# Performance work log

Hardware: AMD Instinct MI355X
Metric: run time of the kernel (lower is better)

## Reference

```python
import jax, jax.numpy as jnp
from jax import lax
import numpy as np

EPS = 1e-4  # ProtoPNet standard epsilon (undefined in simplified source; canonical value)


def setup_inputs() -> dict:
    key = jax.random.key(0)
    k1, k2, k3, k4 = jax.random.split(key, 4)
    B, C_in, H, W = 16, 3, 512, 512
    P, C, NUM_CLASSES = 190, 64, 19
    x = jax.random.normal(k1, (B, C_in, H, W), dtype=jnp.float32)
    feat_w = jax.random.normal(k2, (C, C_in, 7, 7), dtype=jnp.float32) * 0.05  # conv stem, stride 4
    feat_b = jnp.zeros((C,), dtype=jnp.float32)
    prototype_vectors = jax.random.normal(k3, (P, C, 1, 1), dtype=jnp.float32) * 0.1
    last_w = jax.random.normal(k4, (NUM_CLASSES, P), dtype=jnp.float32) * 0.1  # Linear, no bias
    return {"x": x, "feat_w": feat_w, "feat_b": feat_b,
            "prototype_vectors": prototype_vectors, "last_w": last_w}


def reference(x, feat_w, feat_b, prototype_vectors, last_w):
    # features backbone: Conv2d(3->64, k=7, s=4, p=3)
    f = lax.conv_general_dilated(
        x, feat_w, window_strides=(4, 4), padding=[(3, 3), (3, 3)],
        dimension_numbers=("NCHW", "OIHW", "NCHW"))
    f = f + feat_b[None, :, None, None]
    # add_on_layers (deeplab_simple): Sigmoid only
    f = jax.nn.sigmoid(f)  # [B, C, h, w]

    # _l2_convolution with 1x1 prototypes.
    # input_patch_sums = conv(f^2, ones[P,C,1,1]) == sum_c f^2, identical over P -> compute once, broadcast.
    p = prototype_vectors[:, :, 0, 0]                      # [P, C]
    input_patch_sums = jnp.sum(f * f, axis=1, keepdims=True)  # [B, 1, h, w]
    cross_correlation = jnp.einsum("bchw,pc->bphw", f, p)     # [B, P, h, w]
    filter_sums = jnp.sum(p * p, axis=1)[None, :, None, None]  # [1, P, 1, 1]
    distances = input_patch_sums - 2.0 * cross_correlation + filter_sums

    # log activation
    acts = jnp.log((distances + 1.0) / (distances + EPS))  # [B, P, h, w]

    # global max pool over spatial dims, then linear (no bias)
    pooled = jnp.max(acts, axis=(2, 3))                    # [B, P]
    logits = pooled @ last_w.T                             # [B, num_classes]
    return (logits, acts)
```

## Files before the change

### kernel.cpp

```cpp
#include <hip/hip_runtime.h>
#include <hip/hip_bf16.h>


#define N_P   190
#define N_CLS 19
#define N_B   16
#define EPS_F 1e-4f

typedef unsigned short ushort_t;
typedef unsigned int   uint_t;
typedef __attribute__((ext_vector_type(8))) short bf16x8;
typedef __attribute__((ext_vector_type(4))) float f32x4;

__device__ __forceinline__ ushort_t bf16_rne(float v) {
    uint_t u = __float_as_uint(v);
    u += 0x7fffu + ((u >> 16) & 1u);
    return (ushort_t)(u >> 16);
}
__device__ __forceinline__ uint_t pack2(float a, float b) {
    return (uint_t)bf16_rne(a) | ((uint_t)bf16_rne(b) << 16);
}

__global__ void prep_kernel(const float* __restrict__ feat_w,
                            const float* __restrict__ proto,
                            ushort_t* __restrict__ wf,
                            ushort_t* __restrict__ proto_bf,
                            float* __restrict__ fsum) {
    int t = blockIdx.x * 256 + threadIdx.x;
    if (t < 12288) {
        int kr = t >> 9, co = (t >> 3) & 63, kwp = t & 7;
        float v = 0.f;
        if (kr < 21 && kwp >= 1) {
            int ci = kr / 7, kh = kr - ci * 7;
            v = feat_w[co * 147 + ci * 49 + kh * 7 + (kwp - 1)];
        }
        wf[t] = bf16_rne(v);
        int p = t >> 6, c = t & 63;
        proto_bf[t] = bf16_rne((p < N_P) ? proto[p * 64 + c] : 0.f);
    }
    if (t < 192) {
        float s = 0.f;
        if (t < N_P)
            for (int c = 0; c < 64; ++c) {
                float v = proto[t * 64 + c];
                s = fmaf(v, v, s);
            }
        fsum[t] = s;
    }
}

#define XW 520
__global__ __launch_bounds__(256) void conv_kernel(const float* __restrict__ x,
                                                   const ushort_t* __restrict__ wf,
                                                   const float* __restrict__ bias,
                                                   ushort_t* __restrict__ f_bf,
                                                   float* __restrict__ ps) {
    __shared__ ushort_t xs[33 * XW];
    const int b  = blockIdx.x >> 6;
    const int op = blockIdx.x & 63;
    const int tid = threadIdx.x;

    if (tid < 33) *(uint2*)(xs + tid * XW) = make_uint2(0u, 0u);
    const int base_ih = op * 8 - 3;
    for (int i = tid; i < 33 * 128; i += 256) {
        int row = i >> 7;
        int c4  = (i & 127) << 2;
        int ci  = (row * 94) >> 10;
        int ihr = row - ci * 11;
        int ih  = base_ih + ihr;
        float4 v = make_float4(0.f, 0.f, 0.f, 0.f);
        if (ih >= 0 && ih < 512)
            v = *(const float4*)(x + (((b * 3 + ci) * 512 + ih) << 9) + c4);
        uint2 pk = make_uint2(pack2(v.x, v.y), pack2(v.z, v.w));
        *(uint2*)(xs + row * XW + c4 + 4) = pk;
    }
    __syncthreads();

    const int lane = tid & 63, wave = tid >> 6;
    const int n = lane & 15, quad = lane >> 4;
    const int oh_l = wave >> 1, owb = (wave & 1) << 6;

    f32x4 acc[4][4];
#pragma unroll
    for (int ms = 0; ms < 4; ++ms)
#pragma unroll
        for (int ns = 0; ns < 4; ++ns) acc[ms][ns] = (f32x4){0.f, 0.f, 0.f, 0.f};

#pragma unroll
    for (int c = 0; c < 6; ++c) {
        const int kr  = c * 4 + quad;
        const int kra = (kr < 21) ? kr : 0;
        const int ci  = (kra * 37) >> 8;
        const int kh  = kra - ci * 7;
        const ushort_t* bb = xs + (ci * 11 + oh_l * 4 + kh) * XW;

        bf16x8 afr[4], bfr[4];
        const ushort_t* wbase = wf + (kr << 9) + (n << 3);
#pragma unroll
        for (int ms = 0; ms < 4; ++ms)
            afr[ms] = *(const bf16x8*)(wbase + (ms << 7));
#pragma unroll
        for (int ns = 0; ns < 4; ++ns) {
            const ushort_t* p8 = bb + ((owb + ns * 16 + n) << 2);
            union { uint2 u[2]; bf16x8 v; } t2;
            t2.u[0] = *(const uint2*)(p8);
            t2.u[1] = *(const uint2*)(p8 + 4);
            bfr[ns] = t2.v;
        }
#pragma unroll
        for (int ms = 0; ms < 4; ++ms)
#pragma unroll
            for (int ns = 0; ns < 4; ++ns)
                acc[ms][ns] = __builtin_amdgcn_mfma_f32_16x16x32_bf16(
                    afr[ms], bfr[ns], acc[ms][ns], 0, 0, 0);
    }

    const int oh = op * 2 + oh_l;
    const long pixrow = (long)b * 16384 + oh * 128 + owb;
    float psl[4] = {0.f, 0.f, 0.f, 0.f};
#pragma unroll
    for (int ms = 0; ms < 4; ++ms) {
        float4 bv = *(const float4*)(bias + ms * 16 + quad * 4);
        const float* bvp = (const float*)&bv;
#pragma unroll
        for (int ns = 0; ns < 4; ++ns) {
            float fr[4];
#pragma unroll
            for (int r = 0; r < 4; ++r) {
                float z = acc[ms][ns][r] + bvp[r];
                float f = 1.f / (1.f + __expf(-z));
                fr[r] = f;
                psl[ns] = fmaf(f, f, psl[ns]);
            }
            uint2 pk = make_uint2(pack2(fr[0], fr[1]), pack2(fr[2], fr[3]));
            *(uint2*)(f_bf + (pixrow + ns * 16 + n) * 64 + ms * 16 + quad * 4) = pk;
        }
    }
#pragma unroll
    for (int ns = 0; ns < 4; ++ns) {
        float v = psl[ns];
        v += __shfl_xor(v, 16, 64);
        v += __shfl_xor(v, 32, 64);
        if (quad == 0) ps[pixrow + ns * 16 + n] = v;
    }
}

__global__ __launch_bounds__(256) void pp_kernel(const ushort_t* __restrict__ f_bf,
                                                 const float* __restrict__ ps,
                                                 const ushort_t* __restrict__ proto_bf,
                                                 const float* __restrict__ fsum,
                                                 float* __restrict__ acts,
                                                 float* __restrict__ partial) {
    const int b  = blockIdx.x >> 7;
    const int pg = blockIdx.x & 127;
    const int tid = threadIdx.x, lane = tid & 63, wave = tid >> 6;
    const int n = lane & 15, quad = lane >> 4;
    const int wpg = pg * 4 + wave;
    const int pixbase = wpg * 32;
    const long fbase = (long)b * 16384 + pixbase;

    bf16x8 bfr[2][2];
    float psv[2];
#pragma unroll
    for (int s = 0; s < 2; ++s) {
        const ushort_t* fp = f_bf + (fbase + s * 16 + n) * 64 + quad * 8;
        bfr[s][0] = *(const bf16x8*)fp;
        bfr[s][1] = *(const bf16x8*)(fp + 32);
        psv[s] = ps[fbase + s * 16 + n];
    }

    for (int pt = 0; pt < 12; ++pt) {
        const int p0 = pt * 16;
        const ushort_t* ap = proto_bf + (p0 + n) * 64 + quad * 8;
        bf16x8 a0 = *(const bf16x8*)ap;
        bf16x8 a1 = *(const bf16x8*)(ap + 32);
        float4 fsv = *(const float4*)(fsum + p0 + quad * 4);
        const float* fsp = (const float*)&fsv;

        f32x4 acc[2];
#pragma unroll
        for (int s = 0; s < 2; ++s) {
            acc[s] = (f32x4){0.f, 0.f, 0.f, 0.f};
            acc[s] = __builtin_amdgcn_mfma_f32_16x16x32_bf16(a0, bfr[s][0], acc[s], 0, 0, 0);
            acc[s] = __builtin_amdgcn_mfma_f32_16x16x32_bf16(a1, bfr[s][1], acc[s], 0, 0, 0);
        }

        float mx[4] = {-1e30f, -1e30f, -1e30f, -1e30f};
#pragma unroll
        for (int s = 0; s < 2; ++s) {
#pragma unroll
            for (int r = 0; r < 4; ++r) {
                float d = fmaf(-2.f, acc[s][r], psv[s] + fsp[r]);
                float act = __logf(__fdividef(d + 1.f, d + EPS_F));
                mx[r] = fmaxf(mx[r], act);
                int p = p0 + quad * 4 + r;
                if (p < N_P)
                    acts[((long)(b * N_P + p) << 14) + pixbase + s * 16 + n] = act;
            }
        }
#pragma unroll
        for (int r = 0; r < 4; ++r) {
            float m = mx[r];
            m = fmaxf(m, __shfl_xor(m, 1, 64));
            m = fmaxf(m, __shfl_xor(m, 2, 64));
            m = fmaxf(m, __shfl_xor(m, 4, 64));
            m = fmaxf(m, __shfl_xor(m, 8, 64));
            if (n == 0)
                partial[((long)(b * 192 + p0 + quad * 4 + r) << 9) + wpg] = m;
        }
    }
}

__global__ void pool_kernel(const float* __restrict__ partial,
                            float* __restrict__ pooled) {
    const int idx = blockIdx.x;
    const int b = idx / 190, p = idx - b * 190;
    const float4* base = (const float4*)(partial + ((long)(b * 192 + p) << 9));
    const int t = threadIdx.x;
    float4 v0 = base[t * 2], v1 = base[t * 2 + 1];
    float m = fmaxf(fmaxf(fmaxf(v0.x, v0.y), fmaxf(v0.z, v0.w)),
                    fmaxf(fmaxf(v1.x, v1.y), fmaxf(v1.z, v1.w)));
#pragma unroll
    for (int off = 32; off; off >>= 1) m = fmaxf(m, __shfl_xor(m, off, 64));
    if (t == 0) pooled[idx] = m;
}

__global__ void logits_kernel(const float* __restrict__ pooled,
                              const float* __restrict__ last_w,
                              float* __restrict__ logits) {
    int t = blockIdx.x * blockDim.x + threadIdx.x;
    if (t >= N_B * N_CLS) return;
    int b = t / N_CLS, cls = t - b * N_CLS;
    float s = 0.f;
    for (int p = 0; p < N_P; ++p)
        s = fmaf(pooled[b * N_P + p], last_w[cls * N_P + p], s);
    logits[t] = s;
}

extern "C" void kernel_launch(void* const* d_in, const int* in_sizes, int n_in,
                              void* d_out, int out_size, void* d_ws, size_t ws_size,
                              hipStream_t stream) {
    const float* x      = (const float*)d_in[0];
    const float* feat_w = (const float*)d_in[1];
    const float* feat_b = (const float*)d_in[2];
    const float* proto  = (const float*)d_in[3];
    const float* last_w = (const float*)d_in[4];

    float* out_logits = (float*)d_out;
    float* out_acts   = (float*)d_out + N_B * N_CLS;

    char* ws = (char*)d_ws;
    ushort_t* f_bf     = (ushort_t*)(ws);
    float*    ps       = (float*)(ws + 33554432);
    float*    partial  = (float*)(ws + 34603008);
    ushort_t* wf       = (ushort_t*)(ws + 40894464);
    ushort_t* proto_bf = (ushort_t*)(ws + 40919040);
    float*    fsum     = (float*)(ws + 40943616);
    float*    pooled   = (float*)(ws + 40944384);

    prep_kernel<<<48, 256, 0, stream>>>(feat_w, proto, wf, proto_bf, fsum);
    conv_kernel<<<N_B * 64, 256, 0, stream>>>(x, wf, feat_b, f_bf, ps);
    pp_kernel<<<N_B * 128, 256, 0, stream>>>(f_bf, ps, proto_bf, fsum, out_acts, partial);
    pool_kernel<<<N_B * N_P, 64, 0, stream>>>(partial, pooled);
    logits_kernel<<<2, 256, 0, stream>>>(pooled, last_w, out_logits);
}
```

Baseline: 336.8 us.

## Fuse conv stem and prototype distance kernels through swizzled shared memory

Merges the conv+sigmoid kernel with the prototype L2/log-activation kernel. Sigmoid features are staged in bf16 in the reused LDS input buffer, with an XOR swizzle to avoid bank conflicts, and patch sums stay in registers. This removes the global round trip of the bf16 feature map and the separate launch. The cost is more registers per block (4 pixel subtiles of B fragments) and fewer blocks for the distance phase. The partial-max buffer shrinks to match the new per-block pixel tiling.

Measured after the change: 323.6 us. 3.9% less time.

```diff
diff --git a/kernel.cpp b/kernel.cpp
--- a/kernel.cpp
+++ b/kernel.cpp
@@ -50,12 +50,15 @@
 }
 
 #define XW 520
-__global__ __launch_bounds__(256) void conv_kernel(const float* __restrict__ x,
-                                                   const ushort_t* __restrict__ wf,
-                                                   const float* __restrict__ bias,
-                                                   ushort_t* __restrict__ f_bf,
-                                                   float* __restrict__ ps) {
-    __shared__ ushort_t xs[33 * XW];
+__global__ __launch_bounds__(256) void fused_kernel(
+        const float* __restrict__ x,
+        const ushort_t* __restrict__ wf,
+        const float* __restrict__ bias,
+        const ushort_t* __restrict__ proto_bf,
+        const float* __restrict__ fsum,
+        float* __restrict__ acts,
+        float* __restrict__ partial) {
+    __shared__ alignas(16) ushort_t xs[33 * XW];
     const int b  = blockIdx.x >> 6;
     const int op = blockIdx.x & 63;
     const int tid = threadIdx.x;
@@ -115,8 +118,9 @@
                     afr[ms], bfr[ns], acc[ms][ns], 0, 0, 0);
     }
 
-    const int oh = op * 2 + oh_l;
-    const long pixrow = (long)b * 16384 + oh * 128 + owb;
+    __syncthreads();
+
+    char* fls = (char*)xs;
     float psl[4] = {0.f, 0.f, 0.f, 0.f};
 #pragma unroll
     for (int ms = 0; ms < 4; ++ms) {
@@ -132,42 +136,31 @@
                 fr[r] = f;
                 psl[ns] = fmaf(f, f, psl[ns]);
             }
-            uint2 pk = make_uint2(pack2(fr[0], fr[1]), pack2(fr[2], fr[3]));
-            *(uint2*)(f_bf + (pixrow + ns * 16 + n) * 64 + ms * 16 + quad * 4) = pk;
-        }
-    }
+            int pix = wave * 64 + ns * 16 + n;
+            int off = (ms * 32 + quad * 8) ^ ((pix & 7) << 4);
+            *(uint2*)(fls + pix * 128 + off) = make_uint2(pack2(fr[0], fr[1]), pack2(fr[2], fr[3]));
+        }
+    }
+    float psv[4];
 #pragma unroll
     for (int ns = 0; ns < 4; ++ns) {
         float v = psl[ns];
         v += __shfl_xor(v, 16, 64);
         v += __shfl_xor(v, 32, 64);
-        if (quad == 0) ps[pixrow + ns * 16 + n] = v;
-    }
-}
-
-__global__ __launch_bounds__(256) void pp_kernel(const ushort_t* __restrict__ f_bf,
-                                                 const float* __restrict__ ps,
-                                                 const ushort_t* __restrict__ proto_bf,
-                                                 const float* __restrict__ fsum,
-                                                 float* __restrict__ acts,
-                                                 float* __restrict__ partial) {
-    const int b  = blockIdx.x >> 7;
-    const int pg = blockIdx.x & 127;
-    const int tid = threadIdx.x, lane = tid & 63, wave = tid >> 6;
-    const int n = lane & 15, quad = lane >> 4;
-    const int wpg = pg * 4 + wave;
-    const int pixbase = wpg * 32;
-    const long fbase = (long)b * 16384 + pixbase;
-
-    bf16x8 bfr[2][2];
-    float psv[2];
-#pragma unroll
-    for (int s = 0; s < 2; ++s) {
-        const ushort_t* fp = f_bf + (fbase + s * 16 + n) * 64 + quad * 8;
-        bfr[s][0] = *(const bf16x8*)fp;
-        bfr[s][1] = *(const bf16x8*)(fp + 32);
-        psv[s] = ps[fbase + s * 16 + n];
-    }
+        psv[ns] = v;
+    }
+    __syncthreads();
+
+    bf16x8 bfr2[4][2];
+#pragma unroll
+    for (int s = 0; s < 4; ++s) {
+        int pix = wave * 64 + s * 16 + n;
+        int sw = (pix & 7) << 4;
+        bfr2[s][0] = *(const bf16x8*)(fls + pix * 128 + ((quad * 16) ^ sw));
+        bfr2[s][1] = *(const bf16x8*)(fls + pix * 128 + ((64 + quad * 16) ^ sw));
+    }
+    const int oh = op * 2 + oh_l;
+    const int cb = oh * 128 + owb;
 
     for (int pt = 0; pt < 12; ++pt) {
         const int p0 = pt * 16;
@@ -177,25 +170,20 @@
         float4 fsv = *(const float4*)(fsum + p0 + quad * 4);
         const float* fsp = (const float*)&fsv;
 
-        f32x4 acc[2];
-#pragma unroll
-        for (int s = 0; s < 2; ++s) {
-            acc[s] = (f32x4){0.f, 0.f, 0.f, 0.f};
-            acc[s] = __builtin_amdgcn_mfma_f32_16x16x32_bf16(a0, bfr[s][0], acc[s], 0, 0, 0);
-            acc[s] = __builtin_amdgcn_mfma_f32_16x16x32_bf16(a1, bfr[s][1], acc[s], 0, 0, 0);
-        }
-
         float mx[4] = {-1e30f, -1e30f, -1e30f, -1e30f};
 #pragma unroll
-        for (int s = 0; s < 2; ++s) {
+        for (int s = 0; s < 4; ++s) {
+            f32x4 acc2 = (f32x4){0.f, 0.f, 0.f, 0.f};
+            acc2 = __builtin_amdgcn_mfma_f32_16x16x32_bf16(a0, bfr2[s][0], acc2, 0, 0, 0);
+            acc2 = __builtin_amdgcn_mfma_f32_16x16x32_bf16(a1, bfr2[s][1], acc2, 0, 0, 0);
 #pragma unroll
             for (int r = 0; r < 4; ++r) {
-                float d = fmaf(-2.f, acc[s][r], psv[s] + fsp[r]);
+                float d = fmaf(-2.f, acc2[r], psv[s] + fsp[r]);
                 float act = __logf(__fdividef(d + 1.f, d + EPS_F));
                 mx[r] = fmaxf(mx[r], act);
                 int p = p0 + quad * 4 + r;
                 if (p < N_P)
-                    acts[((long)(b * N_P + p) << 14) + pixbase + s * 16 + n] = act;
+                    acts[((long)(b * N_P + p) << 14) + cb + s * 16 + n] = act;
             }
         }
 #pragma unroll
@@ -206,7 +194,7 @@
             m = fmaxf(m, __shfl_xor(m, 4, 64));
             m = fmaxf(m, __shfl_xor(m, 8, 64));
             if (n == 0)
-                partial[((long)(b * 192 + p0 + quad * 4 + r) << 9) + wpg] = m;
+                partial[((long)(b * 192 + p0 + quad * 4 + r) << 8) + op * 4 + wave] = m;
         }
     }
 }
@@ -215,11 +203,10 @@
                             float* __restrict__ pooled) {
     const int idx = blockIdx.x;
     const int b = idx / 190, p = idx - b * 190;
-    const float4* base = (const float4*)(partial + ((long)(b * 192 + p) << 9));
+    const float4* base = (const float4*)(partial + ((long)(b * 192 + p) << 8));
     const int t = threadIdx.x;
-    float4 v0 = base[t * 2], v1 = base[t * 2 + 1];
-    float m = fmaxf(fmaxf(fmaxf(v0.x, v0.y), fmaxf(v0.z, v0.w)),
-                    fmaxf(fmaxf(v1.x, v1.y), fmaxf(v1.z, v1.w)));
+    float4 v0 = base[t];
+    float m = fmaxf(fmaxf(v0.x, v0.y), fmaxf(v0.z, v0.w));
 #pragma unroll
     for (int off = 32; off; off >>= 1) m = fmaxf(m, __shfl_xor(m, off, 64));
     if (t == 0) pooled[idx] = m;
@@ -250,17 +237,14 @@
     float* out_acts   = (float*)d_out + N_B * N_CLS;
 
     char* ws = (char*)d_ws;
-    ushort_t* f_bf     = (ushort_t*)(ws);
-    float*    ps       = (float*)(ws + 33554432);
-    float*    partial  = (float*)(ws + 34603008);
-    ushort_t* wf       = (ushort_t*)(ws + 40894464);
-    ushort_t* proto_bf = (ushort_t*)(ws + 40919040);
-    float*    fsum     = (float*)(ws + 40943616);
-    float*    pooled   = (float*)(ws + 40944384);
+    float*    partial  = (float*)(ws);
+    ushort_t* wf       = (ushort_t*)(ws + 3145728);
+    ushort_t* proto_bf = (ushort_t*)(ws + 3170304);
+    float*    fsum     = (float*)(ws + 3194880);
+    float*    pooled   = (float*)(ws + 3195648);
 
     prep_kernel<<<48, 256, 0, stream>>>(feat_w, proto, wf, proto_bf, fsum);
-    conv_kernel<<<N_B * 64, 256, 0, stream>>>(x, wf, feat_b, f_bf, ps);
-    pp_kernel<<<N_B * 128, 256, 0, stream>>>(f_bf, ps, proto_bf, fsum, out_acts, partial);
+    fused_kernel<<<N_B * 64, 256, 0, stream>>>(x, wf, feat_b, proto_bf, fsum, out_acts, partial);
     pool_kernel<<<N_B * N_P, 64, 0, stream>>>(partial, pooled);
     logits_kernel<<<2, 256, 0, stream>>>(pooled, last_w, out_logits);
 }
```
